# Optimization experiments

Hardware: AMD Instinct MI355X
Metric: run time of the kernel (lower is better)

## Reference

```python
import jax, jax.numpy as jnp
import numpy as np

N_NODES = 100000
N_EDGES = 1600000
DIMS = [100, 200, 128, 128]
EPS = 1e-5


def setup_inputs() -> dict:
    key = jax.random.key(0)
    ks = jax.random.split(key, 32)
    inp = {
        "x": jax.random.normal(ks[0], (N_NODES, DIMS[0]), dtype=jnp.float32),
        "edge_row": jnp.sort(jax.random.randint(ks[1], (N_EDGES,), 0, N_NODES, dtype=jnp.int32)),
        "edge_col": jax.random.randint(ks[2], (N_EDGES,), 0, N_NODES, dtype=jnp.int32),
        "edge_val": jax.random.uniform(ks[3], (N_EDGES,), dtype=jnp.float32),
    }
    # GCwithself layer params: neighbor-agg linear W,b and self linear Ws,bs
    ki = 4
    for i in range(3):
        fi, fo = DIMS[i], DIMS[i + 1]
        s = 1.0 / np.sqrt(fi)
        inp[f"gc{i}_W"] = jax.random.uniform(ks[ki], (fi, fo), minval=-s, maxval=s); ki += 1
        inp[f"gc{i}_b"] = jnp.zeros((fo,), jnp.float32)
        inp[f"gc{i}_Ws"] = jax.random.uniform(ks[ki], (fi, fo), minval=-s, maxval=s); ki += 1
        inp[f"gc{i}_bs"] = jnp.zeros((fo,), jnp.float32)
    s = 1.0 / np.sqrt(128)
    inp["fc1_W"] = jax.random.uniform(ks[ki], (128, 128), minval=-s, maxval=s); ki += 1
    inp["fc1_b"] = jnp.zeros((128,), jnp.float32)
    inp["fc2a_W"] = jax.random.uniform(ks[ki], (128, 256), minval=-s, maxval=s); ki += 1
    inp["fc2a_b"] = jnp.zeros((256,), jnp.float32)
    inp["bn_g"] = jnp.ones((256,), jnp.float32)
    inp["bn_b"] = jnp.zeros((256,), jnp.float32)
    s2 = 1.0 / np.sqrt(256)
    inp["fc2b_W"] = jax.random.uniform(ks[ki], (256, 18), minval=-s2, maxval=s2); ki += 1
    inp["fc2b_b"] = jnp.zeros((18,), jnp.float32)
    return inp


def _gc_layer(x, row, col, val, W, b, Ws, bs):
    # spmm: (adj @ x) via gather + segment-sum, then linear + self-linear + ReLU
    agg = jax.ops.segment_sum(val[:, None] * x[col], row, num_segments=N_NODES)
    return jax.nn.relu(agg @ W + b + x @ Ws + bs)


def _batchnorm(h, g, b):
    mu = jnp.mean(h, axis=0)
    var = jnp.var(h, axis=0)
    return (h - mu) * jax.lax.rsqrt(var + EPS) * g + b


def reference(x, edge_row, edge_col, edge_val,
              gc0_W, gc0_b, gc0_Ws, gc0_bs,
              gc1_W, gc1_b, gc1_Ws, gc1_bs,
              gc2_W, gc2_b, gc2_Ws, gc2_bs,
              fc1_W, fc1_b, fc2a_W, fc2a_b, bn_g, bn_b, fc2b_W, fc2b_b):
    h = _gc_layer(x, edge_row, edge_col, edge_val, gc0_W, gc0_b, gc0_Ws, gc0_bs)
    h = _gc_layer(h, edge_row, edge_col, edge_val, gc1_W, gc1_b, gc1_Ws, gc1_bs)
    h = _gc_layer(h, edge_row, edge_col, edge_val, gc2_W, gc2_b, gc2_Ws, gc2_bs)
    h = jax.nn.relu(h @ fc1_W + fc1_b)
    h = _batchnorm(h @ fc2a_W + fc2a_b, bn_g, bn_b)
    h = jax.nn.relu(h)
    return h @ fc2b_W + fc2b_b
```

## Files before the change

kernel.cpp:

```cpp
#include <hip/hip_runtime.h>

#define N_NODES 100000
#define N_EDGES 1600000

typedef __attribute__((ext_vector_type(8))) short bf16x8;
typedef __attribute__((ext_vector_type(4))) float f32x4;

__device__ __forceinline__ unsigned short f2bf(float f) {
    unsigned u = __float_as_uint(f);
    u = (u + 0x7FFFu + ((u >> 16) & 1u)) >> 16;
    return (unsigned short)u;
}
__device__ __forceinline__ float bf2f(unsigned short h) {
    return __uint_as_float(((unsigned)h) << 16);
}
__device__ __forceinline__ float bflo(unsigned w) { return __uint_as_float(w << 16); }
__device__ __forceinline__ float bfhi(unsigned w) { return __uint_as_float(w & 0xFFFF0000u); }

__device__ __forceinline__ bf16x8 ld_frag(const unsigned short* p) {
    return *(const bf16x8*)p;
}

__global__ void build_row_ptr(const int* __restrict__ row, int* __restrict__ rp) {
    int n = blockIdx.x * blockDim.x + threadIdx.x;
    if (n > N_NODES) return;
    int lo = 0, hi = N_EDGES;
    while (lo < hi) {
        int mid = (lo + hi) >> 1;
        if (row[mid] < n) lo = mid + 1; else hi = mid;
    }
    rp[n] = lo;
}

__global__ __launch_bounds__(256) void conv_x(const float* __restrict__ x,
                                              unsigned short* __restrict__ xb) {
    const int total = N_NODES * 104;
    for (int i = blockIdx.x * 256 + threadIdx.x; i < total; i += gridDim.x * 256) {
        int r = i / 104, c = i - r * 104;
        xb[i] = (c < 100) ? f2bf(x[(size_t)r * 100 + c]) : (unsigned short)0;
    }
}

__global__ __launch_bounds__(256) void prep_all(
    const float* __restrict__ gc0W, const float* __restrict__ gc0Ws,
    const float* __restrict__ gc1W, const float* __restrict__ gc1Ws,
    const float* __restrict__ gc2W, const float* __restrict__ gc2Ws,
    const float* __restrict__ f1W,  const float* __restrict__ f2aW,
    const float* __restrict__ f2bW,
    const float* __restrict__ gc0b, const float* __restrict__ gc0bs,
    const float* __restrict__ gc2b, const float* __restrict__ gc2bs,
    const float* __restrict__ gc1b, const float* __restrict__ gc1bs,
    unsigned short* __restrict__ Bt0, unsigned short* __restrict__ Bt1,
    unsigned short* __restrict__ Bt2, unsigned short* __restrict__ Btf1,
    unsigned short* __restrict__ Btf2a, unsigned short* __restrict__ Btf2b,
    float* __restrict__ bias0, float* __restrict__ bias2, float* __restrict__ bias1)
{
    int i = blockIdx.x * 256 + threadIdx.x;
    if (i < 44800) {
        int n = i / 224, k = i - n * 224; float v = 0.f;
        if (k < 104) { if (k < 100) v = gc0W[(size_t)k * 200 + n]; }
        else { int kr = k - 104; if (kr < 100) v = gc0Ws[(size_t)kr * 200 + n]; }
        Bt0[i] = f2bf(v); return;
    }
    i -= 44800;
    if (i < 57344) {
        int n = i / 224, k = i - n * 224; float v = 0.f;
        if (k < 200) v = (n < 128) ? gc1W[(size_t)k * 128 + n] : gc1Ws[(size_t)k * 128 + (n - 128)];
        Bt1[i] = f2bf(v); return;
    }
    i -= 57344;
    if (i < 32768) {
        int n = i / 256, k = i - n * 256; float v;
        if (k < 128) v = gc2W[(size_t)k * 128 + n];
        else         v = gc2Ws[(size_t)(k - 128) * 128 + n];
        Bt2[i] = f2bf(v); return;
    }
    i -= 32768;
    if (i < 16384) { int n = i >> 7, k = i & 127; Btf1[i] = f2bf(f1W[(size_t)k * 128 + n]); return; }
    i -= 16384;
    if (i < 32768) { int n = i >> 7, k = i & 127; Btf2a[i] = f2bf(f2aW[(size_t)k * 256 + n]); return; }
    i -= 32768;
    if (i < 4608) { int n = i >> 8, k = i & 255; Btf2b[i] = f2bf(f2bW[(size_t)k * 18 + n]); return; }
    i -= 4608;
    if (i < 200) { bias0[i] = gc0b[i] + gc0bs[i]; return; }
    i -= 200;
    if (i < 128) { bias2[i] = gc2b[i] + gc2bs[i]; return; }
    i -= 128;
    if (i < 128) { bias1[i] = gc1b[i] + gc1bs[i]; return; }
}

template<int FUSE>
__global__ __launch_bounds__(256) void spmm_v4(
    const unsigned short* __restrict__ xin, int ldin, int F,
    const int* __restrict__ rp, const int* __restrict__ col,
    const float* __restrict__ val, const float* __restrict__ b01,
    unsigned short* __restrict__ outp, int ldout)
{
    const int node = blockIdx.x * 16 + (threadIdx.x >> 4);
    const int l16 = threadIdx.x & 15;
    const int f8 = l16 * 8;
    const bool act = f8 < F;
    const int e0 = rp[node], e1 = rp[node + 1];
    const unsigned short* xf = xin + f8;

    float a[8];
#pragma unroll
    for (int k = 0; k < 8; k++) a[k] = 0.f;

    for (int e = e0; e < e1; e += 4) {
        int   cj[4]; float vj[4];
#pragma unroll
        for (int j = 0; j < 4; j++) {
            int ej = e + j;
            bool m = ej < e1;
            int es = m ? ej : e0;
            cj[j] = col[es];
            float vv = val[es];
            vj[j] = m ? vv : 0.f;
        }
        if (act) {
#pragma unroll
            for (int j = 0; j < 4; j++) {
                uint4 u = *(const uint4*)(xf + (size_t)cj[j] * ldin);
                float v = vj[j];
                a[0] += v * bflo(u.x); a[1] += v * bfhi(u.x);
                a[2] += v * bflo(u.y); a[3] += v * bfhi(u.y);
                a[4] += v * bflo(u.z); a[5] += v * bfhi(u.z);
                a[6] += v * bflo(u.w); a[7] += v * bfhi(u.w);
            }
        }
    }

    if (act) {
        if (FUSE) {
            uint4 uz = *(const uint4*)(xin + (size_t)node * ldin + 128 + f8);
            float z[8] = {bflo(uz.x), bfhi(uz.x), bflo(uz.y), bfhi(uz.y),
                          bflo(uz.z), bfhi(uz.z), bflo(uz.w), bfhi(uz.w)};
#pragma unroll
            for (int k = 0; k < 8; k++)
                a[k] = fmaxf(a[k] + z[k] + b01[f8 + k], 0.f);
        }
        uint4 pk;
        pk.x = ((unsigned)f2bf(a[1]) << 16) | (unsigned)f2bf(a[0]);
        pk.y = ((unsigned)f2bf(a[3]) << 16) | (unsigned)f2bf(a[2]);
        pk.z = ((unsigned)f2bf(a[5]) << 16) | (unsigned)f2bf(a[4]);
        pk.w = ((unsigned)f2bf(a[7]) << 16) | (unsigned)f2bf(a[6]);
        *(uint4*)(outp + (size_t)node * ldout + f8) = pk;
    }
}

__global__ __launch_bounds__(256) void gemm_head(
    const unsigned short* __restrict__ agg0, const unsigned short* __restrict__ xb,
    const unsigned short* __restrict__ Bt0, const float* __restrict__ bias0,
    const unsigned short* __restrict__ Bt1,
    unsigned short* __restrict__ yz, int M)
{
    __shared__ __align__(16) unsigned short H[64][264];

    const int tid = threadIdx.x;
    const int rowBase = blockIdx.x * 64;
    const int wave = tid >> 6, lane = tid & 63;
    const int cb = wave * 64;
    const int lrow = lane & 15, lq = lane >> 4;
    const int kq = lq * 8;

    {
        f32x4 acc[4][4] = {};
        for (int kk = 0; kk < 224; kk += 32) {
            int k0 = kk + kq;
            bf16x8 af[4], bfr[4];
#pragma unroll
            for (int m = 0; m < 4; ++m) {
                int gr = rowBase + 16 * m + lrow;
                bf16x8 t = {};
                if (gr < M && k0 < 208)
                    t = (k0 < 104) ? ld_frag(agg0 + (size_t)gr * 104 + k0)
                                   : ld_frag(xb   + (size_t)gr * 104 + (k0 - 104));
                af[m] = t;
            }
#pragma unroll
            for (int n = 0; n < 4; ++n) {
                int nr = cb + 16 * n + lrow;
                bf16x8 t = {};
                if (nr < 200) t = ld_frag(Bt0 + (size_t)nr * 224 + k0);
                bfr[n] = t;
            }
#pragma unroll
            for (int m = 0; m < 4; ++m)
#pragma unroll
                for (int n = 0; n < 4; ++n)
                    acc[m][n] = __builtin_amdgcn_mfma_f32_16x16x32_bf16(af[m], bfr[n], acc[m][n], 0, 0, 0);
        }
#pragma unroll
        for (int n = 0; n < 4; ++n) {
            int colg = cb + 16 * n + lrow;
            if (colg >= 224) continue;
            float bb = (colg < 200) ? bias0[colg] : 0.f;
#pragma unroll
            for (int m = 0; m < 4; ++m)
#pragma unroll
                for (int r = 0; r < 4; ++r) {
                    int rowl = 16 * m + lq * 4 + r;
                    H[rowl][colg] = f2bf(fmaxf(acc[m][n][r] + bb, 0.f));
                }
        }
    }
    __syncthreads();

    {
        f32x4 acc[4][4] = {};
        for (int kk = 0; kk < 224; kk += 32) {
            int k0 = kk + kq;
            bf16x8 af[4], bfr[4];
#pragma unroll
            for (int m = 0; m < 4; ++m) af[m] = *(const bf16x8*)&H[16 * m + lrow][k0];
#pragma unroll
            for (int n = 0; n < 4; ++n)
                bfr[n] = ld_frag(Bt1 + (size_t)(cb + 16 * n + lrow) * 224 + k0);
#pragma unroll
            for (int m = 0; m < 4; ++m)
#pragma unroll
                for (int n = 0; n < 4; ++n)
                    acc[m][n] = __builtin_amdgcn_mfma_f32_16x16x32_bf16(af[m], bfr[n], acc[m][n], 0, 0, 0);
        }
        __syncthreads();
#pragma unroll
        for (int n = 0; n < 4; ++n) {
            int colg = cb + 16 * n + lrow;
#pragma unroll
            for (int m = 0; m < 4; ++m)
#pragma unroll
                for (int r = 0; r < 4; ++r) {
                    int rowl = 16 * m + lq * 4 + r;
                    H[rowl][colg] = f2bf(acc[m][n][r]);
                }
        }
    }
    __syncthreads();
#pragma unroll
    for (int i = 0; i < 8; ++i) {
        int c = tid + 256 * i;
        int row = c >> 5;
        int ch  = c & 31;
        int rowg = rowBase + row;
        if (rowg < M)
            *(uint4*)(yz + (size_t)rowg * 256 + ch * 8) = *(const uint4*)&H[row][ch * 8];
    }
}

__global__ __launch_bounds__(256) void gemm_tail(
    const unsigned short* __restrict__ agg2, const unsigned short* __restrict__ h1,
    const unsigned short* __restrict__ Bt2, const float* __restrict__ bias2,
    const unsigned short* __restrict__ Btf1, const float* __restrict__ fc1b,
    const unsigned short* __restrict__ Btf2a, const float* __restrict__ fc2ab,
    unsigned short* __restrict__ h4, float* __restrict__ stats, int M)
{
    __shared__ __align__(16) unsigned short H[64][264];

    const int tid = threadIdx.x;
    const int rowBase = blockIdx.x * 64;
    const int wave = tid >> 6, lane = tid & 63;
    const int lrow = lane & 15, lq = lane >> 4;
    const int kq = lq * 8;

    {
        const int cb = wave * 32;
        f32x4 acc[4][2] = {};
        for (int kk = 0; kk < 256; kk += 32) {
            int k0 = kk + kq;
            const unsigned short* Asrc = (kk < 128) ? agg2 : h1;
            int krel = (kk < 128) ? k0 : k0 - 128;
            bf16x8 af[4], bfr[2];
#pragma unroll
            for (int m = 0; m < 4; ++m) {
                int gr = rowBase + 16 * m + lrow;
                bf16x8 t = {};
                if (gr < M) t = ld_frag(Asrc + (size_t)gr * 128 + krel);
                af[m] = t;
            }
#pragma unroll
            for (int n = 0; n < 2; ++n)
                bfr[n] = ld_frag(Bt2 + (size_t)(cb + 16 * n + lrow) * 256 + k0);
#pragma unroll
            for (int m = 0; m < 4; ++m)
#pragma unroll
                for (int n = 0; n < 2; ++n)
                    acc[m][n] = __builtin_amdgcn_mfma_f32_16x16x32_bf16(af[m], bfr[n], acc[m][n], 0, 0, 0);
        }
#pragma unroll
        for (int n = 0; n < 2; ++n) {
            int colg = cb + 16 * n + lrow;
            float bb = bias2[colg];
#pragma unroll
            for (int m = 0; m < 4; ++m)
#pragma unroll
                for (int r = 0; r < 4; ++r) {
                    int rowl = 16 * m + lq * 4 + r;
                    H[rowl][colg] = f2bf(fmaxf(acc[m][n][r] + bb, 0.f));
                }
        }
    }
    __syncthreads();

    {
        const int cb = wave * 32;
        f32x4 acc[4][2] = {};
        for (int kk = 0; kk < 128; kk += 32) {
            int k0 = kk + kq;
            bf16x8 af[4], bfr[2];
#pragma unroll
            for (int m = 0; m < 4; ++m) af[m] = *(const bf16x8*)&H[16 * m + lrow][k0];
#pragma unroll
            for (int n = 0; n < 2; ++n)
                bfr[n] = ld_frag(Btf1 + (size_t)(cb + 16 * n + lrow) * 128 + k0);
#pragma unroll
            for (int m = 0; m < 4; ++m)
#pragma unroll
                for (int n = 0; n < 2; ++n)
                    acc[m][n] = __builtin_amdgcn_mfma_f32_16x16x32_bf16(af[m], bfr[n], acc[m][n], 0, 0, 0);
        }
        __syncthreads();
#pragma unroll
        for (int n = 0; n < 2; ++n) {
            int colg = cb + 16 * n + lrow;
            float bb = fc1b[colg];
#pragma unroll
            for (int m = 0; m < 4; ++m)
#pragma unroll
                for (int r = 0; r < 4; ++r) {
                    int rowl = 16 * m + lq * 4 + r;
                    H[rowl][colg] = f2bf(fmaxf(acc[m][n][r] + bb, 0.f));
                }
        }
    }
    __syncthreads();

    {
        const int cb = wave * 64;
        f32x4 acc[4][4] = {};
        for (int kk = 0; kk < 128; kk += 32) {
            int k0 = kk + kq;
            bf16x8 af[4], bfr[4];
#pragma unroll
            for (int m = 0; m < 4; ++m) af[m] = *(const bf16x8*)&H[16 * m + lrow][k0];
#pragma unroll
            for (int n = 0; n < 4; ++n)
                bfr[n] = ld_frag(Btf2a + (size_t)(cb + 16 * n + lrow) * 128 + k0);
#pragma unroll
            for (int m = 0; m < 4; ++m)
#pragma unroll
                for (int n = 0; n < 4; ++n)
                    acc[m][n] = __builtin_amdgcn_mfma_f32_16x16x32_bf16(af[m], bfr[n], acc[m][n], 0, 0, 0);
        }
        __syncthreads();

#pragma unroll
        for (int n = 0; n < 4; ++n) {
            int colg = cb + 16 * n + lrow;
            float bb = fc2ab[colg];
            float s = 0.f, s2 = 0.f;
#pragma unroll
            for (int m = 0; m < 4; ++m)
#pragma unroll
                for (int r = 0; r < 4; ++r) {
                    int rowl = 16 * m + lq * 4 + r;
                    float v = acc[m][n][r] + bb;
                    H[rowl][colg] = f2bf(v);
                    if (rowBase + rowl < M) { s += v; s2 += v * v; }
                }
            s  += __shfl_xor(s, 16);  s  += __shfl_xor(s, 32);
            s2 += __shfl_xor(s2, 16); s2 += __shfl_xor(s2, 32);
            if (lq == 0) {
                atomicAdd(&stats[colg], s);
                atomicAdd(&stats[256 + colg], s2);
            }
        }
        __syncthreads();
#pragma unroll
        for (int i = 0; i < 8; ++i) {
            int c = tid + 256 * i;
            int row = c >> 5;
            int ch  = c & 31;
            int rowg = rowBase + row;
            if (rowg < M)
                *(uint4*)(h4 + (size_t)rowg * 256 + ch * 8) = *(const uint4*)&H[row][ch * 8];
        }
    }
}

__global__ void bn_finalize(float* __restrict__ stats,
                            const float* __restrict__ g,
                            const float* __restrict__ b) {
    int t = threadIdx.x;
    const float invN = 1.f / (float)N_NODES;
    float mu = stats[t] * invN;
    float var = stats[256 + t] * invN - mu * mu;
    float sc = g[t] * rsqrtf(var + 1e-5f);
    stats[512 + t] = sc;
    stats[768 + t] = b[t] - mu * sc;
}

__global__ __launch_bounds__(256) void fc2b_kernel(
    const unsigned short* __restrict__ h4, const unsigned short* __restrict__ Btf2b,
    const float* __restrict__ bias, const float* __restrict__ stats,
    float* __restrict__ out, int M)
{
    const int tid = threadIdx.x;
    const int wave = tid >> 6, lane = tid & 63;
    const int lrow = lane & 15, lq = lane >> 4;
    const int kq = lq * 8;
    const int rowBase = blockIdx.x * 128 + wave * 32;

    f32x4 acc[2][2] = {};
    for (int kk = 0; kk < 256; kk += 32) {
        int k0 = kk + kq;
        const float* sc = stats + 512 + k0;
        const float* sh = stats + 768 + k0;
        bf16x8 af[2], bfr[2];
#pragma unroll
        for (int m = 0; m < 2; ++m) {
            int gr = rowBase + 16 * m + lrow;
            uint4 u = make_uint4(0, 0, 0, 0);
            if (gr < M) u = *(const uint4*)(h4 + (size_t)gr * 256 + k0);
            unsigned w[4] = {u.x, u.y, u.z, u.w};
#pragma unroll
            for (int j = 0; j < 4; j++) {
                float lo = fmaxf(bflo(w[j]) * sc[2 * j] + sh[2 * j], 0.f);
                float hi = fmaxf(bfhi(w[j]) * sc[2 * j + 1] + sh[2 * j + 1], 0.f);
                w[j] = ((unsigned)f2bf(hi) << 16) | (unsigned)f2bf(lo);
            }
            uint4 packed = make_uint4(w[0], w[1], w[2], w[3]);
            af[m] = *(const bf16x8*)&packed;
        }
#pragma unroll
        for (int n = 0; n < 2; ++n) {
            int nr = 16 * n + lrow;
            bf16x8 t = {};
            if (nr < 18) t = ld_frag(Btf2b + (size_t)nr * 256 + k0);
            bfr[n] = t;
        }
#pragma unroll
        for (int m = 0; m < 2; ++m)
#pragma unroll
            for (int n = 0; n < 2; ++n)
                acc[m][n] = __builtin_amdgcn_mfma_f32_16x16x32_bf16(af[m], bfr[n], acc[m][n], 0, 0, 0);
    }
#pragma unroll
    for (int n = 0; n < 2; ++n) {
        int colg = 16 * n + lrow;
        if (colg >= 18) continue;
        float bb = bias[colg];
#pragma unroll
        for (int m = 0; m < 2; ++m)
#pragma unroll
            for (int r = 0; r < 4; ++r) {
                int rowg = rowBase + 16 * m + lq * 4 + r;
                if (rowg < M)
                    out[(size_t)rowg * 18 + colg] = acc[m][n][r] + bb;
            }
    }
}

extern "C" void kernel_launch(void* const* d_in, const int* in_sizes, int n_in,
                              void* d_out, int out_size, void* d_ws, size_t ws_size,
                              hipStream_t stream) {
    const float* x        = (const float*)d_in[0];
    const int*   edge_row = (const int*)  d_in[1];
    const int*   edge_col = (const int*)  d_in[2];
    const float* edge_val = (const float*)d_in[3];
    const float* gc0_W  = (const float*)d_in[4];
    const float* gc0_b  = (const float*)d_in[5];
    const float* gc0_Ws = (const float*)d_in[6];
    const float* gc0_bs = (const float*)d_in[7];
    const float* gc1_W  = (const float*)d_in[8];
    const float* gc1_b  = (const float*)d_in[9];
    const float* gc1_Ws = (const float*)d_in[10];
    const float* gc1_bs = (const float*)d_in[11];
    const float* gc2_W  = (const float*)d_in[12];
    const float* gc2_b  = (const float*)d_in[13];
    const float* gc2_Ws = (const float*)d_in[14];
    const float* gc2_bs = (const float*)d_in[15];
    const float* fc1_W  = (const float*)d_in[16];
    const float* fc1_b  = (const float*)d_in[17];
    const float* fc2a_W = (const float*)d_in[18];
    const float* fc2a_b = (const float*)d_in[19];
    const float* bn_g   = (const float*)d_in[20];
    const float* bn_b   = (const float*)d_in[21];
    const float* fc2b_W = (const float*)d_in[22];
    const float* fc2b_b = (const float*)d_in[23];
    float* out = (float*)d_out;

    char* ws = (char*)d_ws;
    int*   rowptr = (int*)ws;
    float* stats  = (float*)(ws + 512 * 1024);
    size_t o = 520 * 1024;
    unsigned short* Bt0   = (unsigned short*)(ws + o); o += 200 * 224 * 2;
    unsigned short* Bt1   = (unsigned short*)(ws + o); o += 256 * 224 * 2;
    unsigned short* Bt2   = (unsigned short*)(ws + o); o += 128 * 256 * 2;
    unsigned short* Btf1  = (unsigned short*)(ws + o); o += 128 * 128 * 2;
    unsigned short* Btf2a = (unsigned short*)(ws + o); o += 256 * 128 * 2;
    unsigned short* Btf2b = (unsigned short*)(ws + o); o += 18 * 256 * 2;
    float* bias0 = (float*)(ws + o); o += 200 * 4;
    float* bias2 = (float*)(ws + o); o += 128 * 4;
    float* bias1 = (float*)(ws + o); o += 128 * 4;
    const size_t SLOT = 52u * 1024 * 1024;
    char* S1 = ws + 1 * 1024 * 1024;
    char* S2 = S1 + SLOT;
    char* S3 = S2 + SLOT;

    unsigned short* xb   = (unsigned short*)S1;
    unsigned short* agg0 = (unsigned short*)S2;
    unsigned short* yz   = (unsigned short*)S3;
    unsigned short* h1   = (unsigned short*)S1;
    unsigned short* agg2 = (unsigned short*)S2;
    unsigned short* h4   = (unsigned short*)S3;

    build_row_ptr<<<392, 256, 0, stream>>>(edge_row, rowptr);
    conv_x<<<2048, 256, 0, stream>>>(x, xb);
    prep_all<<<(189128 + 255) / 256, 256, 0, stream>>>(
        gc0_W, gc0_Ws, gc1_W, gc1_Ws, gc2_W, gc2_Ws, fc1_W, fc2a_W, fc2b_W,
        gc0_b, gc0_bs, gc2_b, gc2_bs, gc1_b, gc1_bs,
        Bt0, Bt1, Bt2, Btf1, Btf2a, Btf2b, bias0, bias2, bias1);
    hipMemsetAsync(stats, 0, 512 * sizeof(float), stream);

    const int spmmGrid = N_NODES / 16;
    const int tile64 = (N_NODES + 63) / 64;

    spmm_v4<0><<<spmmGrid, 256, 0, stream>>>(xb, 104, 104, rowptr, edge_col, edge_val,
                                             nullptr, agg0, 104);
    gemm_head<<<tile64, 256, 0, stream>>>(agg0, xb, Bt0, bias0, Bt1, yz, N_NODES);
    spmm_v4<1><<<spmmGrid, 256, 0, stream>>>(yz, 256, 128, rowptr, edge_col, edge_val,
                                             bias1, h1, 128);
    spmm_v4<0><<<spmmGrid, 256, 0, stream>>>(h1, 128, 128, rowptr, edge_col, edge_val,
                                             nullptr, agg2, 128);
    gemm_tail<<<tile64, 256, 0, stream>>>(
        agg2, h1, Bt2, bias2, Btf1, fc1_b, Btf2a, fc2a_b, h4, stats, N_NODES);
    bn_finalize<<<1, 256, 0, stream>>>(stats, bn_g, bn_b);
    fc2b_kernel<<<(N_NODES + 127) / 128, 256, 0, stream>>>(
        h4, Btf2b, fc2b_b, stats, out, N_NODES);
}
```

Measured before the change: 506.9 us.

## Prefetch GEMM operands and replace BN stat atomics with per-tile partials

In gemm_tail, all B-weight fragments for each stage are preloaded into registers and the A fragments of the first GEMM are double-buffered, so global loads overlap with MFMA work. The per-column atomicAdd accumulation of batchnorm sums is replaced by per-block partial writes into a scratch buffer, and a new bn_reduce kernel (one block per channel) sums them and computes scale and shift. This removes the memset and the atomic contention, but raises register pressure and adds a reduction pass over about 1563 partials per channel.

```diff
diff --git a/kernel.cpp b/kernel.cpp
--- a/kernel.cpp
+++ b/kernel.cpp
@@ -2,6 +2,10 @@
 
 #define N_NODES 100000
 #define N_EDGES 1600000
+#define NTILE64 1563
+#define LDP 1568
+
+#define MEMFENCE asm volatile("" ::: "memory")
 
 typedef __attribute__((ext_vector_type(8))) short bf16x8;
 typedef __attribute__((ext_vector_type(4))) float f32x4;
@@ -253,7 +257,7 @@
     const unsigned short* __restrict__ Bt2, const float* __restrict__ bias2,
     const unsigned short* __restrict__ Btf1, const float* __restrict__ fc1b,
     const unsigned short* __restrict__ Btf2a, const float* __restrict__ fc2ab,
-    unsigned short* __restrict__ h4, float* __restrict__ stats, int M)
+    unsigned short* __restrict__ h4, float* __restrict__ P, int M)
 {
     __shared__ __align__(16) unsigned short H[64][264];
 
@@ -266,26 +270,44 @@
     {
         const int cb = wave * 32;
         f32x4 acc[4][2] = {};
-        for (int kk = 0; kk < 256; kk += 32) {
-            int k0 = kk + kq;
-            const unsigned short* Asrc = (kk < 128) ? agg2 : h1;
-            int krel = (kk < 128) ? k0 : k0 - 128;
-            bf16x8 af[4], bfr[2];
-#pragma unroll
-            for (int m = 0; m < 4; ++m) {
-                int gr = rowBase + 16 * m + lrow;
-                bf16x8 t = {};
-                if (gr < M) t = ld_frag(Asrc + (size_t)gr * 128 + krel);
-                af[m] = t;
-            }
+        bf16x8 Bf[8][2];
+#pragma unroll
+        for (int ki = 0; ki < 8; ++ki)
 #pragma unroll
             for (int n = 0; n < 2; ++n)
-                bfr[n] = ld_frag(Bt2 + (size_t)(cb + 16 * n + lrow) * 256 + k0);
+                Bf[ki][n] = ld_frag(Bt2 + (size_t)(cb + 16 * n + lrow) * 256 + 32 * ki + kq);
+        MEMFENCE;
+        bf16x8 A2[2][4];
+#pragma unroll
+        for (int m = 0; m < 4; ++m) {
+            int gr = rowBase + 16 * m + lrow;
+            bf16x8 t = {};
+            if (gr < M) t = ld_frag(agg2 + (size_t)gr * 128 + kq);
+            A2[0][m] = t;
+        }
+        MEMFENCE;
+#pragma unroll
+        for (int ki = 0; ki < 8; ++ki) {
+            const int cur = ki & 1;
+            if (ki < 7) {
+                const int kin = ki + 1;
+                int k0 = 32 * kin + kq;
+                const unsigned short* Asrc = (kin < 4) ? agg2 : h1;
+                int krel = (kin < 4) ? k0 : k0 - 128;
+#pragma unroll
+                for (int m = 0; m < 4; ++m) {
+                    int gr = rowBase + 16 * m + lrow;
+                    bf16x8 t = {};
+                    if (gr < M) t = ld_frag(Asrc + (size_t)gr * 128 + krel);
+                    A2[cur ^ 1][m] = t;
+                }
+            }
+            MEMFENCE;
 #pragma unroll
             for (int m = 0; m < 4; ++m)
 #pragma unroll
                 for (int n = 0; n < 2; ++n)
-                    acc[m][n] = __builtin_amdgcn_mfma_f32_16x16x32_bf16(af[m], bfr[n], acc[m][n], 0, 0, 0);
+                    acc[m][n] = __builtin_amdgcn_mfma_f32_16x16x32_bf16(A2[cur][m], Bf[ki][n], acc[m][n], 0, 0, 0);
         }
 #pragma unroll
         for (int n = 0; n < 2; ++n) {
@@ -305,19 +327,23 @@
     {
         const int cb = wave * 32;
         f32x4 acc[4][2] = {};
-        for (int kk = 0; kk < 128; kk += 32) {
-            int k0 = kk + kq;
-            bf16x8 af[4], bfr[2];
-#pragma unroll
-            for (int m = 0; m < 4; ++m) af[m] = *(const bf16x8*)&H[16 * m + lrow][k0];
+        bf16x8 Bf[4][2];
+#pragma unroll
+        for (int ki = 0; ki < 4; ++ki)
 #pragma unroll
             for (int n = 0; n < 2; ++n)
-                bfr[n] = ld_frag(Btf1 + (size_t)(cb + 16 * n + lrow) * 128 + k0);
+                Bf[ki][n] = ld_frag(Btf1 + (size_t)(cb + 16 * n + lrow) * 128 + 32 * ki + kq);
+        MEMFENCE;
+#pragma unroll
+        for (int ki = 0; ki < 4; ++ki) {
+            bf16x8 af[4];
+#pragma unroll
+            for (int m = 0; m < 4; ++m) af[m] = *(const bf16x8*)&H[16 * m + lrow][32 * ki + kq];
 #pragma unroll
             for (int m = 0; m < 4; ++m)
 #pragma unroll
                 for (int n = 0; n < 2; ++n)
-                    acc[m][n] = __builtin_amdgcn_mfma_f32_16x16x32_bf16(af[m], bfr[n], acc[m][n], 0, 0, 0);
+                    acc[m][n] = __builtin_amdgcn_mfma_f32_16x16x32_bf16(af[m], Bf[ki][n], acc[m][n], 0, 0, 0);
         }
         __syncthreads();
 #pragma unroll
@@ -338,19 +364,23 @@
     {
         const int cb = wave * 64;
         f32x4 acc[4][4] = {};
-        for (int kk = 0; kk < 128; kk += 32) {
-            int k0 = kk + kq;
-            bf16x8 af[4], bfr[4];
-#pragma unroll
-            for (int m = 0; m < 4; ++m) af[m] = *(const bf16x8*)&H[16 * m + lrow][k0];
+        bf16x8 Bf[4][4];
+#pragma unroll
+        for (int ki = 0; ki < 4; ++ki)
 #pragma unroll
             for (int n = 0; n < 4; ++n)
-                bfr[n] = ld_frag(Btf2a + (size_t)(cb + 16 * n + lrow) * 128 + k0);
+                Bf[ki][n] = ld_frag(Btf2a + (size_t)(cb + 16 * n + lrow) * 128 + 32 * ki + kq);
+        MEMFENCE;
+#pragma unroll
+        for (int ki = 0; ki < 4; ++ki) {
+            bf16x8 af[4];
+#pragma unroll
+            for (int m = 0; m < 4; ++m) af[m] = *(const bf16x8*)&H[16 * m + lrow][32 * ki + kq];
 #pragma unroll
             for (int m = 0; m < 4; ++m)
 #pragma unroll
                 for (int n = 0; n < 4; ++n)
-                    acc[m][n] = __builtin_amdgcn_mfma_f32_16x16x32_bf16(af[m], bfr[n], acc[m][n], 0, 0, 0);
+                    acc[m][n] = __builtin_amdgcn_mfma_f32_16x16x32_bf16(af[m], Bf[ki][n], acc[m][n], 0, 0, 0);
         }
         __syncthreads();
 
@@ -371,8 +401,8 @@
             s  += __shfl_xor(s, 16);  s  += __shfl_xor(s, 32);
             s2 += __shfl_xor(s2, 16); s2 += __shfl_xor(s2, 32);
             if (lq == 0) {
-                atomicAdd(&stats[colg], s);
-                atomicAdd(&stats[256 + colg], s2);
+                P[(size_t)colg * LDP + blockIdx.x] = s;
+                P[(size_t)(256 + colg) * LDP + blockIdx.x] = s2;
             }
         }
         __syncthreads();
@@ -388,16 +418,32 @@
     }
 }
 
-__global__ void bn_finalize(float* __restrict__ stats,
-                            const float* __restrict__ g,
-                            const float* __restrict__ b) {
-    int t = threadIdx.x;
-    const float invN = 1.f / (float)N_NODES;
-    float mu = stats[t] * invN;
-    float var = stats[256 + t] * invN - mu * mu;
-    float sc = g[t] * rsqrtf(var + 1e-5f);
-    stats[512 + t] = sc;
-    stats[768 + t] = b[t] - mu * sc;
+__global__ __launch_bounds__(256) void bn_reduce(const float* __restrict__ P,
+                                                 const float* __restrict__ g,
+                                                 const float* __restrict__ b,
+                                                 float* __restrict__ stats) {
+    const int c = blockIdx.x;
+    const int tid = threadIdx.x;
+    __shared__ float r1[256], r2[256];
+    float s = 0.f, s2 = 0.f;
+    for (int i = tid; i < NTILE64; i += 256) {
+        s  += P[(size_t)c * LDP + i];
+        s2 += P[(size_t)(256 + c) * LDP + i];
+    }
+    r1[tid] = s; r2[tid] = s2;
+    __syncthreads();
+    for (int off = 128; off > 0; off >>= 1) {
+        if (tid < off) { r1[tid] += r1[tid + off]; r2[tid] += r2[tid + off]; }
+        __syncthreads();
+    }
+    if (tid == 0) {
+        const float invN = 1.f / (float)N_NODES;
+        float mu = r1[0] * invN;
+        float var = r2[0] * invN - mu * mu;
+        float sc = g[c] * rsqrtf(var + 1e-5f);
+        stats[512 + c] = sc;
+        stats[768 + c] = b[c] - mu * sc;
+    }
 }
 
 __global__ __launch_bounds__(256) void fc2b_kernel(
@@ -514,6 +560,7 @@
     unsigned short* h1   = (unsigned short*)S1;
     unsigned short* agg2 = (unsigned short*)S2;
     unsigned short* h4   = (unsigned short*)S3;
+    float* Pp = (float*)(S2 + 40u * 1024 * 1024);
 
     build_row_ptr<<<392, 256, 0, stream>>>(edge_row, rowptr);
     conv_x<<<2048, 256, 0, stream>>>(x, xb);
@@ -521,21 +568,19 @@
         gc0_W, gc0_Ws, gc1_W, gc1_Ws, gc2_W, gc2_Ws, fc1_W, fc2a_W, fc2b_W,
         gc0_b, gc0_bs, gc2_b, gc2_bs, gc1_b, gc1_bs,
         Bt0, Bt1, Bt2, Btf1, Btf2a, Btf2b, bias0, bias2, bias1);
-    hipMemsetAsync(stats, 0, 512 * sizeof(float), stream);
 
     const int spmmGrid = N_NODES / 16;
-    const int tile64 = (N_NODES + 63) / 64;
 
     spmm_v4<0><<<spmmGrid, 256, 0, stream>>>(xb, 104, 104, rowptr, edge_col, edge_val,
                                              nullptr, agg0, 104);
-    gemm_head<<<tile64, 256, 0, stream>>>(agg0, xb, Bt0, bias0, Bt1, yz, N_NODES);
+    gemm_head<<<NTILE64, 256, 0, stream>>>(agg0, xb, Bt0, bias0, Bt1, yz, N_NODES);
     spmm_v4<1><<<spmmGrid, 256, 0, stream>>>(yz, 256, 128, rowptr, edge_col, edge_val,
                                              bias1, h1, 128);
     spmm_v4<0><<<spmmGrid, 256, 0, stream>>>(h1, 128, 128, rowptr, edge_col, edge_val,
                                              nullptr, agg2, 128);
-    gemm_tail<<<tile64, 256, 0, stream>>>(
-        agg2, h1, Bt2, bias2, Btf1, fc1_b, Btf2a, fc2a_b, h4, stats, N_NODES);
-    bn_finalize<<<1, 256, 0, stream>>>(stats, bn_g, bn_b);
+    gemm_tail<<<NTILE64, 256, 0, stream>>>(
+        agg2, h1, Bt2, bias2, Btf1, fc1_b, Btf2a, fc2a_b, h4, Pp, N_NODES);
+    bn_reduce<<<256, 256, 0, stream>>>(Pp, bn_g, bn_b, stats);
     fc2b_kernel<<<(N_NODES + 127) / 128, 256, 0, stream>>>(
         h4, Btf2b, fc2b_b, stats, out, N_NODES);
 }
```

Result: faster. 490.0 us (-3.3%).
